# Optimization experiments

Hardware: AMD Instinct MI355X
Metric: run time of the kernel (lower is better)

## Reference

```python
import math
import jax, jax.numpy as jnp
import numpy as np

H = 1024      # d_model
NHALF = 32    # N // 2
L_LEN = 4096
DT_MIN, DT_MAX = 1e-3, 1e-1


def setup_inputs() -> dict:
    key = jax.random.key(0)
    k1, k2 = jax.random.split(key)
    # C stored as real view of a complex (H, N/2) tensor -> (H, N/2, 2)
    C_ri = jax.random.normal(k1, (H, NHALF, 2), dtype=jnp.float32)
    # log_dt ~ Uniform(log(dt_min), log(dt_max))
    u = jax.random.uniform(k2, (H,), dtype=jnp.float32)
    log_dt = u * (math.log(DT_MAX) - math.log(DT_MIN)) + math.log(DT_MIN)
    # log_A_real = log(0.5 * ones), A_imag = pi * arange(N/2) broadcast over H
    log_A_real = jnp.full((H, NHALF), math.log(0.5), dtype=jnp.float32)
    A_imag = math.pi * jnp.broadcast_to(jnp.arange(NHALF, dtype=jnp.float32), (H, NHALF))
    A_imag = jnp.asarray(A_imag)
    return {"C_ri": C_ri, "log_dt": log_dt, "log_A_real": log_A_real,
            "A_imag": A_imag, "L": L_LEN}


def reference(C_ri, log_dt, log_A_real, A_imag, L):
    dt = jnp.exp(log_dt)                              # (H,)
    C = C_ri[..., 0] + 1j * C_ri[..., 1]              # (H, n) complex
    A = -jnp.exp(log_A_real) + 1j * A_imag            # (H, n) complex
    dtA = A * dt[:, None]                             # (H, n)
    # Vandermonde: exp(dtA * l) for l in [0, L)  -> (H, n, L) complex
    coeffs = dtA[:, :, None] * jnp.arange(L, dtype=jnp.float32)
    lhs = C * (jnp.exp(dtA) - 1.0) / A                # (H, n)
    K_complex = jnp.einsum('hn,hnl->hl', lhs, jnp.exp(coeffs))
    return 2.0 * K_complex.real                       # (H, L) float32
```

## Files before the change

### kernel.cpp

```cpp
#include <hip/hip_runtime.h>
#include <math.h>

#define HDIM 1024
#define NH 32
#define LLEN 4096
#define NT 512
#define LDK 72

typedef __attribute__((ext_vector_type(8))) short bf16x8;
typedef __attribute__((ext_vector_type(4))) float f32x4;

__device__ __forceinline__ unsigned int fbits(float x) { return __builtin_bit_cast(unsigned int, x); }
__device__ __forceinline__ float bitsf(unsigned int u) { return __builtin_bit_cast(float, u); }

__global__ __launch_bounds__(NT, 4) void s4d_kernel(
    const float* __restrict__ C_ri,
    const float* __restrict__ log_dt,
    const float* __restrict__ log_A_real,
    const float* __restrict__ A_imag,
    float* __restrict__ out)
{
    __shared__ unsigned short sAh[64][LDK], sAl[64][LDK];
    __shared__ unsigned short sBh[64][LDK], sBl[64][LDK];

    const int h = blockIdx.x;
    const int tid = threadIdx.x;
    const int n = tid & 31;
    const int hn = h * NH + n;
    const int r0 = tid >> 5;

    const float LOG2E = 1.4426950408889634f;

    const float dt = exp2f(log_dt[h] * LOG2E);
    const float Ar = -exp2f(log_A_real[hn] * LOG2E);
    const float Ai = A_imag[hn];
    const float dtAr = Ar * dt;
    const float dtAi = Ai * dt;
    const float re2 = dtAr * LOG2E;

    const double sd = (double)dtAi * 0.15915494309189535;
    const double fdd = sd - floor(sd);
    const float phi = (float)(floor(fdd * 4096.0 + 0.5) * (1.0 / 4096.0));
    const float plo = (float)(fdd - (double)phi);

    const float er = exp2f(re2);
    const float rv = (float)fdd;
    const float cs = __builtin_amdgcn_cosf(rv);
    const float sn = __builtin_amdgcn_sinf(rv);
    const float Er = er * cs - 1.0f;
    const float Ei = er * sn;
    const float cr = C_ri[2 * hn + 0];
    const float ci = C_ri[2 * hn + 1];
    const float nr = cr * Er - ci * Ei;
    const float ni = cr * Ei + ci * Er;
    const float inv = 1.0f / (Ar * Ar + Ai * Ai);
    const float lr = (nr * Ar + ni * Ai) * inv;
    const float li = (ni * Ar - nr * Ai) * inv;

    auto zpow = [&](float m, float& zr, float& zi) {
        const float x = phi * m;
        const float fr = x - floorf(x);
        float rev = fmaf(plo, m, fr);
        rev -= floorf(rev);
        const float ev = exp2f(re2 * m);
        zr = ev * __builtin_amdgcn_cosf(rev);
        zi = ev * __builtin_amdgcn_sinf(rev);
    };

    {
        float zr, zi, sr, si;
        zpow((float)r0, zr, zi);
        zpow(16.0f, sr, si);
        int row = r0;
#pragma unroll
        for (int k = 0; k < 4; ++k) {
            const unsigned int urb = fbits(zr), uib = fbits(zi);
            const unsigned int hp = (urb >> 16) | (uib & 0xFFFF0000u);
            const float rl = zr - bitsf(urb & 0xFFFF0000u);
            const float il = zi - bitsf(uib & 0xFFFF0000u);
            const unsigned int lp = (fbits(rl) >> 16) | (fbits(il) & 0xFFFF0000u);
            *(unsigned int*)&sAh[row][2 * n] = hp;
            *(unsigned int*)&sAl[row][2 * n] = lp;
            const float t = zr * sr - zi * si;
            zi = zr * si + zi * sr;
            zr = t;
            row += 16;
        }
    }

    {
        float zr, zi, sr, si;
        zpow((float)(64 * r0), zr, zi);
        zpow(1024.0f, sr, si);
        float ur = lr * zr - li * zi;
        float ui = lr * zi + li * zr;
        int row = r0;
#pragma unroll
        for (int k = 0; k < 4; ++k) {
            const float br = ur + ur;
            const float bi = -(ui + ui);
            const unsigned int urb = fbits(br), uib = fbits(bi);
            const unsigned int hp = (urb >> 16) | (uib & 0xFFFF0000u);
            const float rl = br - bitsf(urb & 0xFFFF0000u);
            const float il = bi - bitsf(uib & 0xFFFF0000u);
            const unsigned int lp = (fbits(rl) >> 16) | (fbits(il) & 0xFFFF0000u);
            *(unsigned int*)&sBh[row][2 * n] = hp;
            *(unsigned int*)&sBl[row][2 * n] = lp;
            const float t = ur * sr - ui * si;
            ui = ur * si + ui * sr;
            ur = t;
            row += 16;
        }
    }
    __syncthreads();

    const int wv = tid >> 6;
    const int lane = tid & 63;
    const int li16 = lane & 15;
    const int lg = lane >> 4;
    const int arow = wv & 3;
    const int tc0 = (wv >> 2) * 2;

    f32x4 acc[2];
    acc[0] = (f32x4){0.f, 0.f, 0.f, 0.f};
    acc[1] = (f32x4){0.f, 0.f, 0.f, 0.f};

#pragma unroll
    for (int s = 0; s < 6; ++s) {
        const unsigned short (*Am)[LDK] = (s >= 4) ? sAl : sAh;
        const unsigned short (*Bm)[LDK] = (s == 2 || s == 3) ? sBl : sBh;
        const int ko = (s & 1) * 32 + 8 * lg;
        const bf16x8 af = *(const bf16x8*)&Am[16 * arow + li16][ko];
#pragma unroll
        for (int t = 0; t < 2; ++t) {
            const bf16x8 bfr = *(const bf16x8*)&Bm[16 * (tc0 + t) + li16][ko];
            acc[t] = __builtin_amdgcn_mfma_f32_16x16x32_bf16(af, bfr, acc[t], 0, 0, 0);
        }
    }

    const int rr = 16 * arow + 4 * lg;
#pragma unroll
    for (int t = 0; t < 2; ++t) {
        const int q = 16 * (tc0 + t) + li16;
        *(f32x4*)&out[h * LLEN + 64 * q + rr] = acc[t];
    }
}

extern "C" void kernel_launch(void* const* d_in, const int* in_sizes, int n_in,
                              void* d_out, int out_size, void* d_ws, size_t ws_size,
                              hipStream_t stream) {
    const float* C_ri       = (const float*)d_in[0];
    const float* log_dt     = (const float*)d_in[1];
    const float* log_A_real = (const float*)d_in[2];
    const float* A_imag     = (const float*)d_in[3];
    float* out = (float*)d_out;

    s4d_kernel<<<dim3(HDIM), dim3(NT), 0, stream>>>(C_ri, log_dt, log_A_real, A_imag, out);
}
```

Measured before the change: 12.66 us.

## Process two heads per block with XOR-swizzled shared tables and overlapped build/GEMM

Halves the grid to 512 blocks so each block handles two heads, double-buffering the shared-memory tables so the second head's table build can overlap the first head's MFMA and store. Replaces the padded LDK=72 layout with an XOR swizzle on 64-wide rows to avoid bank conflicts. Aims to cut launch/tail overhead and hide setup latency, but the per-block serial chain gets longer, shared memory use doubles, and there are fewer blocks to spread across the CUs.

```diff
diff --git a/kernel.cpp b/kernel.cpp
--- a/kernel.cpp
+++ b/kernel.cpp
@@ -5,7 +5,7 @@
 #define NH 32
 #define LLEN 4096
 #define NT 512
-#define LDK 72
+#define NBLK 512
 
 typedef __attribute__((ext_vector_type(8))) short bf16x8;
 typedef __attribute__((ext_vector_type(4))) float f32x4;
@@ -13,37 +13,29 @@
 __device__ __forceinline__ unsigned int fbits(float x) { return __builtin_bit_cast(unsigned int, x); }
 __device__ __forceinline__ float bitsf(unsigned int u) { return __builtin_bit_cast(float, u); }
 
-__global__ __launch_bounds__(NT, 4) void s4d_kernel(
-    const float* __restrict__ C_ri,
-    const float* __restrict__ log_dt,
-    const float* __restrict__ log_A_real,
-    const float* __restrict__ A_imag,
-    float* __restrict__ out)
-{
-    __shared__ unsigned short sAh[64][LDK], sAl[64][LDK];
-    __shared__ unsigned short sBh[64][LDK], sBl[64][LDK];
+struct Setup { float lr, li, re2, phi, plo; };
 
-    const int h = blockIdx.x;
-    const int tid = threadIdx.x;
-    const int n = tid & 31;
+__device__ __forceinline__ Setup make_setup(const float* __restrict__ C_ri,
+                                            const float* __restrict__ log_dt,
+                                            const float* __restrict__ log_A_real,
+                                            const float* __restrict__ A_imag,
+                                            int h, int n) {
     const int hn = h * NH + n;
-    const int r0 = tid >> 5;
-
     const float LOG2E = 1.4426950408889634f;
-
     const float dt = exp2f(log_dt[h] * LOG2E);
     const float Ar = -exp2f(log_A_real[hn] * LOG2E);
     const float Ai = A_imag[hn];
     const float dtAr = Ar * dt;
     const float dtAi = Ai * dt;
-    const float re2 = dtAr * LOG2E;
 
+    Setup s;
+    s.re2 = dtAr * LOG2E;
     const double sd = (double)dtAi * 0.15915494309189535;
     const double fdd = sd - floor(sd);
-    const float phi = (float)(floor(fdd * 4096.0 + 0.5) * (1.0 / 4096.0));
-    const float plo = (float)(fdd - (double)phi);
+    s.phi = (float)(floor(fdd * 4096.0 + 0.5) * (1.0 / 4096.0));
+    s.plo = (float)(fdd - (double)s.phi);
 
-    const float er = exp2f(re2);
+    const float er = exp2f(s.re2);
     const float rv = (float)fdd;
     const float cs = __builtin_amdgcn_cosf(rv);
     const float sn = __builtin_amdgcn_sinf(rv);
@@ -54,17 +46,31 @@
     const float nr = cr * Er - ci * Ei;
     const float ni = cr * Ei + ci * Er;
     const float inv = 1.0f / (Ar * Ar + Ai * Ai);
-    const float lr = (nr * Ar + ni * Ai) * inv;
-    const float li = (ni * Ar - nr * Ai) * inv;
+    s.lr = (nr * Ar + ni * Ai) * inv;
+    s.li = (ni * Ar - nr * Ai) * inv;
+    return s;
+}
 
+__device__ __forceinline__ void build_h(const Setup& s, int n, int r0,
+                                        unsigned short (*T)[64][64]) {
     auto zpow = [&](float m, float& zr, float& zi) {
-        const float x = phi * m;
+        const float x = s.phi * m;
         const float fr = x - floorf(x);
-        float rev = fmaf(plo, m, fr);
+        float rev = fmaf(s.plo, m, fr);
         rev -= floorf(rev);
-        const float ev = exp2f(re2 * m);
+        const float ev = exp2f(s.re2 * m);
         zr = ev * __builtin_amdgcn_cosf(rev);
         zi = ev * __builtin_amdgcn_sinf(rev);
+    };
+    auto put = [&](int tab, int row, float vr, float vi) {
+        const unsigned ur = fbits(vr), ui = fbits(vi);
+        const unsigned hp = (ur >> 16) | (ui & 0xFFFF0000u);
+        const float rl = vr - bitsf(ur & 0xFFFF0000u);
+        const float il = vi - bitsf(ui & 0xFFFF0000u);
+        const unsigned lp = (fbits(rl) >> 16) | (fbits(il) & 0xFFFF0000u);
+        const int c = n ^ ((row & 7) << 2);
+        ((unsigned*)T[tab][row])[c] = hp;
+        ((unsigned*)T[tab + 1][row])[c] = lp;
     };
 
     {
@@ -74,76 +80,88 @@
         int row = r0;
 #pragma unroll
         for (int k = 0; k < 4; ++k) {
-            const unsigned int urb = fbits(zr), uib = fbits(zi);
-            const unsigned int hp = (urb >> 16) | (uib & 0xFFFF0000u);
-            const float rl = zr - bitsf(urb & 0xFFFF0000u);
-            const float il = zi - bitsf(uib & 0xFFFF0000u);
-            const unsigned int lp = (fbits(rl) >> 16) | (fbits(il) & 0xFFFF0000u);
-            *(unsigned int*)&sAh[row][2 * n] = hp;
-            *(unsigned int*)&sAl[row][2 * n] = lp;
+            put(0, row, zr, zi);
             const float t = zr * sr - zi * si;
             zi = zr * si + zi * sr;
             zr = t;
             row += 16;
         }
     }
-
     {
         float zr, zi, sr, si;
         zpow((float)(64 * r0), zr, zi);
         zpow(1024.0f, sr, si);
-        float ur = lr * zr - li * zi;
-        float ui = lr * zi + li * zr;
+        float ur = s.lr * zr - s.li * zi;
+        float ui = s.lr * zi + s.li * zr;
         int row = r0;
 #pragma unroll
         for (int k = 0; k < 4; ++k) {
-            const float br = ur + ur;
-            const float bi = -(ui + ui);
-            const unsigned int urb = fbits(br), uib = fbits(bi);
-            const unsigned int hp = (urb >> 16) | (uib & 0xFFFF0000u);
-            const float rl = br - bitsf(urb & 0xFFFF0000u);
-            const float il = bi - bitsf(uib & 0xFFFF0000u);
-            const unsigned int lp = (fbits(rl) >> 16) | (fbits(il) & 0xFFFF0000u);
-            *(unsigned int*)&sBh[row][2 * n] = hp;
-            *(unsigned int*)&sBl[row][2 * n] = lp;
+            put(2, row, ur + ur, -(ui + ui));
             const float t = ur * sr - ui * si;
             ui = ur * si + ui * sr;
             ur = t;
             row += 16;
         }
     }
-    __syncthreads();
+}
 
+__device__ __forceinline__ void gemm_store(const unsigned short (*T)[64][64],
+                                           int tid, float* __restrict__ outh) {
+    const int lane = tid & 63;
     const int wv = tid >> 6;
-    const int lane = tid & 63;
     const int li16 = lane & 15;
     const int lg = lane >> 4;
     const int arow = wv & 3;
     const int tc0 = (wv >> 2) * 2;
 
-    f32x4 acc[2];
-    acc[0] = (f32x4){0.f, 0.f, 0.f, 0.f};
-    acc[1] = (f32x4){0.f, 0.f, 0.f, 0.f};
+    f32x4 acc0 = (f32x4){0.f, 0.f, 0.f, 0.f};
+    f32x4 acc1 = (f32x4){0.f, 0.f, 0.f, 0.f};
+
+    const int rowA = 16 * arow + li16;
+    const int rowB0 = 16 * tc0 + li16;
+    const int rowB1 = rowB0 + 16;
 
 #pragma unroll
-    for (int s = 0; s < 6; ++s) {
-        const unsigned short (*Am)[LDK] = (s >= 4) ? sAl : sAh;
-        const unsigned short (*Bm)[LDK] = (s == 2 || s == 3) ? sBl : sBh;
-        const int ko = (s & 1) * 32 + 8 * lg;
-        const bf16x8 af = *(const bf16x8*)&Am[16 * arow + li16][ko];
-#pragma unroll
-        for (int t = 0; t < 2; ++t) {
-            const bf16x8 bfr = *(const bf16x8*)&Bm[16 * (tc0 + t) + li16][ko];
-            acc[t] = __builtin_amdgcn_mfma_f32_16x16x32_bf16(af, bfr, acc[t], 0, 0, 0);
-        }
+    for (int st = 0; st < 6; ++st) {
+        const int tabA = (st >= 4) ? 1 : 0;
+        const int tabB = (st == 2 || st == 3) ? 3 : 2;
+        const int j = 4 * (st & 1) + lg;
+        const bf16x8 af = *(const bf16x8*)&T[tabA][rowA][8 * (j ^ (rowA & 7))];
+        const bf16x8 b0 = *(const bf16x8*)&T[tabB][rowB0][8 * (j ^ (rowB0 & 7))];
+        const bf16x8 b1 = *(const bf16x8*)&T[tabB][rowB1][8 * (j ^ (rowB1 & 7))];
+        acc0 = __builtin_amdgcn_mfma_f32_16x16x32_bf16(af, b0, acc0, 0, 0, 0);
+        acc1 = __builtin_amdgcn_mfma_f32_16x16x32_bf16(af, b1, acc1, 0, 0, 0);
     }
 
     const int rr = 16 * arow + 4 * lg;
-#pragma unroll
-    for (int t = 0; t < 2; ++t) {
-        const int q = 16 * (tc0 + t) + li16;
-        *(f32x4*)&out[h * LLEN + 64 * q + rr] = acc[t];
-    }
+    *(f32x4*)&outh[64 * (16 * tc0 + li16) + rr] = acc0;
+    *(f32x4*)&outh[64 * (16 * tc0 + 16 + li16) + rr] = acc1;
+}
+
+__global__ __launch_bounds__(NT, 4) void s4d_kernel(
+    const float* __restrict__ C_ri,
+    const float* __restrict__ log_dt,
+    const float* __restrict__ log_A_real,
+    const float* __restrict__ A_imag,
+    float* __restrict__ out)
+{
+    __shared__ unsigned short sT[2][4][64][64];
+
+    const int tid = threadIdx.x;
+    const int n = tid & 31;
+    const int r0 = tid >> 5;
+    const int h0 = blockIdx.x;
+    const int h1 = blockIdx.x + NBLK;
+
+    const Setup s0 = make_setup(C_ri, log_dt, log_A_real, A_imag, h0, n);
+    const Setup s1 = make_setup(C_ri, log_dt, log_A_real, A_imag, h1, n);
+
+    build_h(s0, n, r0, sT[0]);
+    __syncthreads();
+    gemm_store(sT[0], tid, out + h0 * LLEN);
+    build_h(s1, n, r0, sT[1]);
+    __syncthreads();
+    gemm_store(sT[1], tid, out + h1 * LLEN);
 }
 
 extern "C" void kernel_launch(void* const* d_in, const int* in_sizes, int n_in,
@@ -155,5 +173,5 @@
     const float* A_imag     = (const float*)d_in[3];
     float* out = (float*)d_out;
 
-    s4d_kernel<<<dim3(HDIM), dim3(NT), 0, stream>>>(C_ri, log_dt, log_A_real, A_imag, out);
+    s4d_kernel<<<dim3(NBLK), dim3(NT), 0, stream>>>(C_ri, log_dt, log_A_real, A_imag, out);
 }
```

Result: no change. 12.66 us (median of 2 runs) (-0.0%).
